# Performance work log

Measured on AMD Instinct MI355X. Metric: run time of the kernel, lower is better.

The kernel has to match this reference:

```python
import jax, jax.numpy as jnp
import numpy as np
import math

N_KEYS = 2048      # set size (number of pragma keys)
EMB = 768          # embed_size
KEY_E = 512        # key_embed_size
VAL_E = 256        # val_embed_size (KEY_E + VAL_E == EMB)
CAT_VOCAB = 100000 # categorical embedding rows
N_REG = 1000       # integer-key embedding rows / per-key Linear(1,256) encoders
HID = 512          # hidden_size (dim_V)
HEADS = 8
N_OUT = 7          # PMA num_outputs
SCALE = math.sqrt(HID)  # original divides by sqrt(dim_V), not sqrt(head_dim)


def _split_heads(x):
    # torch: torch.cat(x.split(dim_V//h, 2), 0)  -> [h*B, N, dim_V/h]
    return jnp.concatenate(jnp.split(x, HEADS, axis=2), axis=0)


def _merge_heads(x):
    # torch: torch.cat(x.split(B, 0), 2)
    return jnp.concatenate(jnp.split(x, HEADS, axis=0), axis=2)


def _mab(Q, K, wq, bq, wk, bk, wv, bv, wo, bo):
    # MAB with ln=False: project, head-split along batch, attend, residual, relu FF residual
    Qp = Q @ wq.T + bq
    Kp = K @ wk.T + bk
    Vp = K @ wv.T + bv
    Q_, K_, V_ = _split_heads(Qp), _split_heads(Kp), _split_heads(Vp)
    A = jax.nn.softmax(jnp.einsum('bqd,bkd->bqk', Q_, K_) / SCALE, axis=-1)
    O = _merge_heads(Q_ + jnp.einsum('bqk,bkd->bqd', A, V_))
    return O + jax.nn.relu(O @ wo.T + bo)


def _forward(reg_values, cat_table, reg_table, reg_W, reg_b,
             q0_w, q0_b, k0_w, k0_b, v0_w, v0_b, o0_w, o0_b,
             qs_w, qs_b, ks_w, ks_b, vs_w, vs_b, os_w, os_b,
             S, pq_w, pq_b, pk_w, pk_b, pv_w, pv_b, po_w, po_b,
             fc_w, fc_b, is_cat, cat_idx, reg_idx):
    # vectorized form of the per-key python loop: gather -> tiny linear encode -> select
    val_emb = reg_W[reg_idx] * reg_values[:, None] + reg_b[reg_idx]     # [N, VAL_E]
    reg_full = jnp.concatenate([reg_table[reg_idx], val_emb], axis=-1)  # [N, EMB]
    emb = jnp.where(is_cat[:, None], cat_table[cat_idx], reg_full)[None]  # [1, N, EMB]
    x = _mab(emb, emb, q0_w, q0_b, k0_w, k0_b, v0_w, v0_b, o0_w, o0_b)
    for i in range(3):
        x = _mab(x, x, qs_w[i], qs_b[i], ks_w[i], ks_b[i], vs_w[i], vs_b[i], os_w[i], os_b[i])
    # decoder: PMA (MAB(S, X)) then Linear(HID, 1)
    s = jnp.broadcast_to(S, (x.shape[0], N_OUT, HID))
    p = _mab(s, x, pq_w, pq_b, pk_w, pk_b, pv_w, pv_b, po_w, po_b)      # [1, N_OUT, HID]
    return (p @ fc_w.T + fc_b).reshape(-1)                              # [N_OUT]


def setup_inputs() -> dict:
    key = jax.random.key(0)
    ks = iter(jax.random.split(key, 48))
    def w(shape, s=0.02):
        return jax.random.normal(next(ks), shape, jnp.float32) * s
    inp = {}
    inp['is_cat'] = jax.random.bernoulli(next(ks), 0.5, (N_KEYS,))
    inp['cat_idx'] = jax.random.randint(next(ks), (N_KEYS,), 0, CAT_VOCAB)
    inp['reg_idx'] = jax.random.randint(next(ks), (N_KEYS,), 0, N_REG)
    inp['reg_values'] = jax.random.uniform(next(ks), (N_KEYS,), jnp.float32, 1.0, 64.0)
    inp['cat_table'] = w((CAT_VOCAB, EMB), 0.05)
    inp['reg_table'] = w((N_REG, KEY_E), 0.05)
    inp['reg_W'] = w((N_REG, VAL_E))
    inp['reg_b'] = w((N_REG, VAL_E))
    inp['q0_w'] = w((HID, EMB)); inp['q0_b'] = w((HID,))
    inp['k0_w'] = w((HID, EMB)); inp['k0_b'] = w((HID,))
    inp['v0_w'] = w((HID, EMB)); inp['v0_b'] = w((HID,))
    inp['o0_w'] = w((HID, HID)); inp['o0_b'] = w((HID,))
    for nm in ['qs', 'ks', 'vs', 'os']:
        inp[nm + '_w'] = w((3, HID, HID))
        inp[nm + '_b'] = w((3, HID))
    inp['S'] = w((1, N_OUT, HID), 0.05)
    for nm in ['pq', 'pk', 'pv', 'po']:
        inp[nm + '_w'] = w((HID, HID))
        inp[nm + '_b'] = w((HID,))
    inp['fc_w'] = w((1, HID)); inp['fc_b'] = w((1,))
    return inp


def reference(is_cat, cat_idx, reg_idx, reg_values, cat_table, reg_table, reg_W, reg_b,
              q0_w, q0_b, k0_w, k0_b, v0_w, v0_b, o0_w, o0_b,
              qs_w, qs_b, ks_w, ks_b, vs_w, vs_b, os_w, os_b,
              S, pq_w, pq_b, pk_w, pk_b, pv_w, pv_b, po_w, po_b, fc_w, fc_b):
    return _forward(reg_values, cat_table, reg_table, reg_W, reg_b,
                    q0_w, q0_b, k0_w, k0_b, v0_w, v0_b, o0_w, o0_b,
                    qs_w, qs_b, ks_w, ks_b, vs_w, vs_b, os_w, os_b,
                    S, pq_w, pq_b, pk_w, pk_b, pv_w, pv_b, po_w, po_b,
                    fc_w, fc_b, is_cat, cat_idx, reg_idx)
```

## Files before the change

### kernel.cpp

```cpp
#include <hip/hip_runtime.h>
#include <hip/hip_bf16.h>
#include <stdint.h>


#define HID 512
#define EMBD 768
#define NCTX 2048
#define HD 64

typedef __attribute__((ext_vector_type(8))) short v8s;
typedef __attribute__((ext_vector_type(4))) float v4f;

#define MFMA(a, b, c) __builtin_amdgcn_mfma_f32_16x16x32_bf16((a), (b), (c), 0, 0, 0)

__device__ __forceinline__ short f2bf(float f) {
  return __builtin_bit_cast(short, __float2bfloat16(f));
}
__device__ __forceinline__ float bf2f(short s) {
  uint32_t u = ((uint32_t)(uint16_t)s) << 16;
  return __builtin_bit_cast(float, u);
}
__device__ __forceinline__ v8s ldbf8(const short* p) { return *(const v8s*)p; }

struct ConvDesc {
  const float* src[20];
  unsigned cum[21];
};

#define NB_CONV 22016u
#define NB_EMB 6144u
#define NB_S 128u

__global__ __launch_bounds__(256) void k_prep(
    ConvDesc d, short* __restrict__ Wdst,
    const int* __restrict__ is_cat, const int* __restrict__ cat_idx,
    const int* __restrict__ reg_idx, const float* __restrict__ reg_values,
    const float* __restrict__ cat_table, const float* __restrict__ reg_table,
    const float* __restrict__ reg_W, const float* __restrict__ reg_b,
    short* __restrict__ emb_out, const float* __restrict__ S,
    short* __restrict__ s_out) {
  unsigned b = blockIdx.x;
  if (b < NB_CONV) {
    unsigned i = b * 256u + threadIdx.x;
    if (i >= d.cum[20]) return;
    int t = 0;
    while (i >= d.cum[t + 1]) ++t;
    Wdst[i] = f2bf(d.src[t][i - d.cum[t]]);
  } else if (b < NB_CONV + NB_EMB) {
    int i = (int)(b - NB_CONV) * 256 + threadIdx.x;
    int n = i / EMBD, e = i - n * EMBD;
    float v;
    if (is_cat[n]) {
      v = cat_table[(long)cat_idx[n] * EMBD + e];
    } else {
      int r = reg_idx[n];
      if (e < 512) v = reg_table[r * 512 + e];
      else {
        int e2 = e - 512;
        v = reg_W[r * 256 + e2] * reg_values[n] + reg_b[r * 256 + e2];
      }
    }
    emb_out[i] = f2bf(v);
  } else {
    int i = (int)(b - NB_CONV - NB_EMB) * 256 + threadIdx.x;
    int row = i >> 9;
    s_out[i] = (row < 7) ? f2bf(S[i]) : (short)0;
  }
}

struct GemmJob {
  const short* A;
  const short* B;
  const float* biasA;
  const float* biasB;
  short* out;
  int N, KK, epi, gx, base;
  float sA, sB;
};
struct GemmBatch {
  GemmJob j[3];
  int nj;
};

__global__ __launch_bounds__(64) void k_gemm_multi(GemmBatch gb) {
  int wg = blockIdx.x;
  int ji = 0;
  if (gb.nj > 1 && wg >= gb.j[1].base) ji = 1;
  if (gb.nj > 2 && wg >= gb.j[2].base) ji = 2;
  const GemmJob& j = gb.j[ji];
  int rel = wg - j.base;
  int bx = rel % j.gx, by = rel / j.gx;
  int l = threadIdx.x, l16 = l & 15, quad = l >> 4;
  int i0 = by * 32, n0 = bx * 64;
  const int KK = j.KK;
  const short* a0p = j.A + (i0 + l16) * KK + quad * 8;
  const short* a1p = a0p + 16 * KK;
  const short* bp = j.B + (n0 + l16) * KK + quad * 8;
  v4f acc[2][4];
  for (int g = 0; g < 2; ++g)
    for (int t = 0; t < 4; ++t) acc[g][t] = (v4f){0.f, 0.f, 0.f, 0.f};
#pragma unroll 4
  for (int k = 0; k < KK; k += 32) {
    v8s a0 = ldbf8(a0p + k);
    v8s a1 = ldbf8(a1p + k);
#pragma unroll
    for (int t = 0; t < 4; ++t) {
      v8s b = ldbf8(bp + t * 16 * KK + k);
      acc[0][t] = MFMA(a0, b, acc[0][t]);
      acc[1][t] = MFMA(a1, b, acc[1][t]);
    }
  }
  for (int g = 0; g < 2; ++g)
    for (int t = 0; t < 4; ++t) {
      int col = n0 + t * 16 + l16;
      float bc = 0.f, sc = 1.f;
      if (j.epi == 0) {
        bc = (col < 512) ? j.biasA[col] : j.biasB[col - 512];
        sc = (col < 512) ? j.sA : j.sB;
      }
      for (int r = 0; r < 4; ++r) {
        int row = i0 + g * 16 + quad * 4 + r;
        float v = acc[g][t][r];
        v = (j.epi == 0) ? (v + bc) * sc : v + j.biasA[row];
        j.out[row * j.N + col] = f2bf(v);
      }
    }
}

template <int KK>
__global__ __launch_bounds__(64) void k_gemm_ff(const short* __restrict__ A,
                                               const short* __restrict__ B,
                                               const float* __restrict__ biasA,
                                               const short* __restrict__ resid,
                                               short* __restrict__ out, int N) {
  int l = threadIdx.x, l16 = l & 15, quad = l >> 4;
  int i0 = blockIdx.y * 32, n0 = blockIdx.x * 64;
  const short* a0p = A + (i0 + l16) * KK + quad * 8;
  const short* a1p = a0p + 16 * KK;
  const short* bp = B + (n0 + l16) * KK + quad * 8;
  v4f acc[2][4];
  for (int g = 0; g < 2; ++g)
    for (int t = 0; t < 4; ++t) acc[g][t] = (v4f){0.f, 0.f, 0.f, 0.f};
#pragma unroll 4
  for (int k = 0; k < KK; k += 32) {
    v8s a0 = ldbf8(a0p + k);
    v8s a1 = ldbf8(a1p + k);
#pragma unroll
    for (int t = 0; t < 4; ++t) {
      v8s b = ldbf8(bp + t * 16 * KK + k);
      acc[0][t] = MFMA(a0, b, acc[0][t]);
      acc[1][t] = MFMA(a1, b, acc[1][t]);
    }
  }
  for (int g = 0; g < 2; ++g)
    for (int t = 0; t < 4; ++t) {
      int col = n0 + t * 16 + l16;
      float bc = biasA[col];
      for (int r = 0; r < 4; ++r) {
        int row = i0 + g * 16 + quad * 4 + r;
        float v = bf2f(resid[row * N + col]) + fmaxf(acc[g][t][r] + bc, 0.f);
        out[row * N + col] = f2bf(v);
      }
    }
}

__global__ __launch_bounds__(256) void k_flash(const short* __restrict__ Q, int qstride,
                                               const short* __restrict__ Kp, int kstride,
                                               const short* __restrict__ Vt,
                                               float* __restrict__ opart,
                                               float* __restrict__ lspart) {
  __shared__ __align__(16) short Kt[64 * 64];
  __shared__ __align__(16) short Vtl[64 * 64];
  __shared__ __align__(16) short P[4][16 * 72];
  const int tid = threadIdx.x;
  const int wave = tid >> 6, l = tid & 63, l16 = l & 15, quad = l >> 4;
  const int h = blockIdx.y, D0 = h * HD;
  const int i0 = blockIdx.x * 64 + wave * 16;
  const int z = blockIdx.z, jbase = z * (NCTX / 4);

  const short* qrow = Q + (i0 + l16) * qstride + D0 + quad * 8;
  const v8s aq0 = ldbf8(qrow);
  const v8s aq1 = ldbf8(qrow + 32);

  const int sr = tid >> 2, sc0 = tid & 3, sc1 = sc0 + 4;
  const short* kg = Kp + (jbase + sr) * kstride + D0;
  const short* vg = Vt + (D0 + sr) * NCTX + jbase;
  short* kl0 = &Kt[(sr * 8 + (sc0 ^ (sr & 7))) * 8];
  short* kl1 = &Kt[(sr * 8 + (sc1 ^ (sr & 7))) * 8];
  short* vl0 = &Vtl[(sr * 8 + (sc0 ^ (sr & 7))) * 8];
  short* vl1 = &Vtl[(sr * 8 + (sc1 ^ (sr & 7))) * 8];

  v4f o[4];
  float lsum[4];
  for (int t = 0; t < 4; ++t) o[t] = (v4f){0.f, 0.f, 0.f, 0.f};
  for (int r = 0; r < 4; ++r) lsum[r] = 0.f;

  v8s pk0 = ldbf8(kg + sc0 * 8), pk1 = ldbf8(kg + sc1 * 8);
  v8s pv0 = ldbf8(vg + sc0 * 8), pv1 = ldbf8(vg + sc1 * 8);

  for (int j0 = 0; j0 < NCTX / 4; j0 += 64) {
    __syncthreads();
    *(v8s*)kl0 = pk0; *(v8s*)kl1 = pk1;
    *(v8s*)vl0 = pv0; *(v8s*)vl1 = pv1;
    __syncthreads();
    int jn = j0 + 64;
    if (jn < NCTX / 4) {
      pk0 = ldbf8(kg + jn * kstride + sc0 * 8);
      pk1 = ldbf8(kg + jn * kstride + sc1 * 8);
      pv0 = ldbf8(vg + jn + sc0 * 8);
      pv1 = ldbf8(vg + jn + sc1 * 8);
    }
    v4f s[4];
#pragma unroll
    for (int kt = 0; kt < 4; ++kt) {
      int R = kt * 16 + l16;
      v8s kb0 = *(const v8s*)&Kt[(R * 8 + (quad ^ (R & 7))) * 8];
      v8s kb1 = *(const v8s*)&Kt[(R * 8 + ((quad + 4) ^ (R & 7))) * 8];
      v4f t0 = (v4f){0.f, 0.f, 0.f, 0.f};
      t0 = MFMA(aq0, kb0, t0);
      s[kt] = MFMA(aq1, kb1, t0);
    }
    short* pw = &P[wave][0];
#pragma unroll
    for (int kt = 0; kt < 4; ++kt)
      for (int r = 0; r < 4; ++r) {
        float p = exp2f(fminf(s[kt][r], 40.f));
        lsum[r] += p;
        pw[(quad * 4 + r) * 72 + kt * 16 + l16] = f2bf(p);
      }
    asm volatile("s_waitcnt lgkmcnt(0)" ::: "memory");
    v8s pa0 = *(const v8s*)&pw[l16 * 72 + quad * 8];
    v8s pa1 = *(const v8s*)&pw[l16 * 72 + 32 + quad * 8];
#pragma unroll
    for (int t = 0; t < 4; ++t) {
      int R = t * 16 + l16;
      v8s bv0 = *(const v8s*)&Vtl[(R * 8 + (quad ^ (R & 7))) * 8];
      v8s bv1 = *(const v8s*)&Vtl[(R * 8 + ((quad + 4) ^ (R & 7))) * 8];
      o[t] = MFMA(pa0, bv0, o[t]);
      o[t] = MFMA(pa1, bv1, o[t]);
    }
  }
  for (int r = 0; r < 4; ++r) {
    lsum[r] += __shfl_xor(lsum[r], 1);
    lsum[r] += __shfl_xor(lsum[r], 2);
    lsum[r] += __shfl_xor(lsum[r], 4);
    lsum[r] += __shfl_xor(lsum[r], 8);
  }
  float* ob = opart + (size_t)z * (NCTX * HID);
  for (int t = 0; t < 4; ++t)
    for (int r = 0; r < 4; ++r)
      ob[(i0 + quad * 4 + r) * HID + D0 + t * 16 + l16] = o[t][r];
  if (l16 == 0)
    for (int r = 0; r < 4; ++r)
      lspart[z * (8 * NCTX) + h * NCTX + i0 + quad * 4 + r] = lsum[r];
}

__global__ void k_combine(const float* __restrict__ op, const float* __restrict__ ls,
                          const short* __restrict__ Qr, int qstride,
                          short* __restrict__ out) {
  const int PS = NCTX * HID;
  int i = blockIdx.x * 256 + threadIdx.x;
  int row = i >> 9, col = i & 511, h = col >> 6;
  float o = op[i] + op[i + PS] + op[i + 2 * PS] + op[i + 3 * PS];
  int li = h * NCTX + row;
  float d = ls[li] + ls[li + 8 * NCTX] + ls[li + 16 * NCTX] + ls[li + 24 * NCTX];
  out[i] = f2bf(bf2f(Qr[row * qstride + col]) + o / d);
}

__global__ __launch_bounds__(64) void k_fc(const short* __restrict__ P,
                                           const float* __restrict__ fcw,
                                           const float* __restrict__ fcb,
                                           float* __restrict__ out) {
  int j = blockIdx.x, l = threadIdx.x;
  float s = 0.f;
  int d0 = l * 8;
  for (int d = d0; d < d0 + 8; ++d) s += bf2f(P[j * HID + d]) * fcw[d];
  for (int msk = 1; msk < 64; msk <<= 1) s += __shfl_xor(s, msk);
  if (l == 0) out[j] = s + fcb[0];
}

extern "C" void kernel_launch(void* const* d_in, const int* in_sizes, int n_in,
                              void* d_out, int out_size, void* d_ws, size_t ws_size,
                              hipStream_t stream) {
  const int* is_cat = (const int*)d_in[0];
  const int* cat_idx = (const int*)d_in[1];
  const int* reg_idx = (const int*)d_in[2];
  const float* reg_values = (const float*)d_in[3];
  const float* cat_table = (const float*)d_in[4];
  const float* reg_table = (const float*)d_in[5];
  const float* reg_W = (const float*)d_in[6];
  const float* reg_b = (const float*)d_in[7];
  const float* q0_w = (const float*)d_in[8];  const float* q0_b = (const float*)d_in[9];
  const float* k0_w = (const float*)d_in[10]; const float* k0_b = (const float*)d_in[11];
  const float* v0_w = (const float*)d_in[12]; const float* v0_b = (const float*)d_in[13];
  const float* o0_w = (const float*)d_in[14]; const float* o0_b = (const float*)d_in[15];
  const float* qs_w = (const float*)d_in[16]; const float* qs_b = (const float*)d_in[17];
  const float* ks_w = (const float*)d_in[18]; const float* ks_b = (const float*)d_in[19];
  const float* vs_w = (const float*)d_in[20]; const float* vs_b = (const float*)d_in[21];
  const float* os_w = (const float*)d_in[22]; const float* os_b = (const float*)d_in[23];
  const float* S    = (const float*)d_in[24];
  const float* pq_w = (const float*)d_in[25]; const float* pq_b = (const float*)d_in[26];
  const float* pk_w = (const float*)d_in[27]; const float* pk_b = (const float*)d_in[28];
  const float* pv_w = (const float*)d_in[29]; const float* pv_b = (const float*)d_in[30];
  const float* po_w = (const float*)d_in[31]; const float* po_b = (const float*)d_in[32];
  const float* fc_w = (const float*)d_in[33]; const float* fc_b = (const float*)d_in[34];

  short* W = (short*)d_ws;

  const unsigned OWQK[4] = {0u, 1441792u, 2490368u, 3538944u};
  const unsigned OWV[4]  = {786432u, 1966080u, 3014656u, 4063232u};
  const unsigned OWO[4]  = {1179648u, 2228224u, 3276800u, 4325376u};
  const unsigned OPQW = 4587520u, OPKW = 4849664u, OPVW = 5111808u, OPOW = 5373952u;
  const unsigned TOTW = 5636096u;
  const unsigned OEMB = TOTW;
  const unsigned OXA  = OEMB + 1572864u;
  const unsigned OXB  = OXA + 1048576u;
  const unsigned OQK  = OXB + 1048576u;
  const unsigned OVT  = OQK + 2097152u;
  const unsigned OOH  = OVT + 1048576u;
  const unsigned OSB  = OOH + 1048576u;
  const unsigned OQPP = OSB + 32768u;
  const unsigned OKPP = OQPP + 32768u;
  const unsigned OOHP = OKPP + 1048576u;
  const unsigned OPP  = OOHP + 32768u;
  const unsigned OF32 = OPP + 32768u;
  float* F = (float*)(W + OF32);
  float* LS = F + 4u * 1048576u;

  const float C2 = 0.06375872f;

  ConvDesc cd;
  const float* srcs[20] = {
      q0_w, k0_w, v0_w, o0_w,
      qs_w, ks_w, vs_w, os_w,
      qs_w + 262144, ks_w + 262144, vs_w + 262144, os_w + 262144,
      qs_w + 524288, ks_w + 524288, vs_w + 524288, os_w + 524288,
      pq_w, pk_w, pv_w, po_w};
  const unsigned cums[21] = {0u,       393216u,  786432u,  1179648u, 1441792u,
                             1703936u, 1966080u, 2228224u, 2490368u, 2752512u,
                             3014656u, 3276800u, 3538944u, 3801088u, 4063232u,
                             4325376u, 4587520u, 4849664u, 5111808u, 5373952u,
                             5636096u};
  for (int i = 0; i < 20; ++i) cd.src[i] = srcs[i];
  for (int i = 0; i < 21; ++i) cd.cum[i] = cums[i];
  k_prep<<<NB_CONV + NB_EMB + NB_S, 256, 0, stream>>>(
      cd, W, is_cat, cat_idx, reg_idx, reg_values, cat_table, reg_table,
      reg_W, reg_b, W + OEMB, S, W + OSB);

  const float* bq[4] = {q0_b, qs_b, qs_b + 512, qs_b + 1024};
  const float* bk[4] = {k0_b, ks_b, ks_b + 512, ks_b + 1024};
  const float* bv[4] = {v0_b, vs_b, vs_b + 512, vs_b + 1024};
  const float* bo[4] = {o0_b, os_b, os_b + 512, os_b + 1024};
  const unsigned oxin[4]  = {OEMB, OXA, OXB, OXA};
  const unsigned oxout[4] = {OXA, OXB, OXA, OXB};

  dim3 gf(32, 8, 4);

  for (int l = 0; l < 4; ++l) {
    const short* X = W + oxin[l];
    short* Xout = W + oxout[l];
    int KKl = (l == 0) ? 768 : 512;
    GemmBatch gb{};
    gb.nj = 2;
    gb.j[0] = {X, W + OWQK[l], bq[l], bk[l], W + OQK, 1024, KKl, 0, 16, 0, 1.f, C2};
    gb.j[1] = {W + OWV[l], X, bv[l], nullptr, W + OVT, 2048, KKl, 1, 32, 1024, 1.f, 1.f};
    k_gemm_multi<<<1536, 64, 0, stream>>>(gb);
    k_flash<<<gf, 256, 0, stream>>>(W + OQK, 1024, W + OQK + 512, 1024, W + OVT, F, LS);
    k_combine<<<(2048 * 512) / 256, 256, 0, stream>>>(F, LS, W + OQK, 1024, W + OOH);
    k_gemm_ff<512><<<dim3(8, 64), 64, 0, stream>>>(W + OOH, W + OWO[l], bo[l], W + OOH, Xout, 512);
  }

  GemmBatch gp{};
  gp.nj = 3;
  gp.j[0] = {W + OSB, W + OPQW, pq_b, pq_b, W + OQPP, 512, 512, 0, 8, 0, 1.f, 1.f};
  gp.j[1] = {W + OXB, W + OPKW, pk_b, pk_b, W + OKPP, 512, 512, 0, 8, 16, C2, C2};
  gp.j[2] = {W + OPVW, W + OXB, pv_b, nullptr, W + OVT, 2048, 512, 1, 32, 528, 1.f, 1.f};
  k_gemm_multi<<<1040, 64, 0, stream>>>(gp);
  k_flash<<<dim3(1, 8, 4), 256, 0, stream>>>(W + OQPP, 512, W + OKPP, 512, W + OVT, F, LS);
  k_combine<<<(16 * 512) / 256, 256, 0, stream>>>(F, LS, W + OQPP, 512, W + OOHP);
  k_gemm_ff<512><<<dim3(8, 1), 64, 0, stream>>>(W + OOHP, W + OPOW, po_b, W + OOHP, W + OPP, 512);
  k_fc<<<7, 64, 0, stream>>>(W + OPP, fc_w, fc_b, (float*)d_out);
}
```

Baseline: 728.0 us.

## Fuse split-K flash combine into flash kernel via last-arriving-block reduction

```diff
diff --git a/kernel.cpp b/kernel.cpp
--- a/kernel.cpp
+++ b/kernel.cpp
@@ -38,7 +38,7 @@
     const float* __restrict__ cat_table, const float* __restrict__ reg_table,
     const float* __restrict__ reg_W, const float* __restrict__ reg_b,
     short* __restrict__ emb_out, const float* __restrict__ S,
-    short* __restrict__ s_out) {
+    short* __restrict__ s_out, int* __restrict__ cnt) {
   unsigned b = blockIdx.x;
   if (b < NB_CONV) {
     unsigned i = b * 256u + threadIdx.x;
@@ -61,10 +61,12 @@
       }
     }
     emb_out[i] = f2bf(v);
-  } else {
+  } else if (b < NB_CONV + NB_EMB + NB_S) {
     int i = (int)(b - NB_CONV - NB_EMB) * 256 + threadIdx.x;
     int row = i >> 9;
     s_out[i] = (row < 7) ? f2bf(S[i]) : (short)0;
+  } else {
+    for (int k = 0; k < 8; ++k) cnt[threadIdx.x * 8 + k] = 0;
   }
 }
 
@@ -168,10 +170,13 @@
                                                const short* __restrict__ Kp, int kstride,
                                                const short* __restrict__ Vt,
                                                float* __restrict__ opart,
-                                               float* __restrict__ lspart) {
+                                               float* __restrict__ lspart,
+                                               int* __restrict__ cnt,
+                                               short* __restrict__ oout) {
   __shared__ __align__(16) short Kt[64 * 64];
   __shared__ __align__(16) short Vtl[64 * 64];
   __shared__ __align__(16) short P[4][16 * 72];
+  __shared__ int arrival;
   const int tid = threadIdx.x;
   const int wave = tid >> 6, l = tid & 63, l16 = l & 15, quad = l >> 4;
   const int h = blockIdx.y, D0 = h * HD;
@@ -253,18 +258,34 @@
   if (l16 == 0)
     for (int r = 0; r < 4; ++r)
       lspart[z * (8 * NCTX) + h * NCTX + i0 + quad * 4 + r] = lsum[r];
-}
-
-__global__ void k_combine(const float* __restrict__ op, const float* __restrict__ ls,
-                          const short* __restrict__ Qr, int qstride,
-                          short* __restrict__ out) {
-  const int PS = NCTX * HID;
-  int i = blockIdx.x * 256 + threadIdx.x;
-  int row = i >> 9, col = i & 511, h = col >> 6;
-  float o = op[i] + op[i + PS] + op[i + 2 * PS] + op[i + 3 * PS];
-  int li = h * NCTX + row;
-  float d = ls[li] + ls[li + 8 * NCTX] + ls[li + 16 * NCTX] + ls[li + 24 * NCTX];
-  out[i] = f2bf(bf2f(Qr[row * qstride + col]) + o / d);
+
+  __threadfence();
+  __syncthreads();
+  if (tid == 0) arrival = atomicAdd(&cnt[blockIdx.y * gridDim.x + blockIdx.x], 1);
+  __syncthreads();
+  if (arrival != 3) return;
+  __threadfence();
+
+  float dtot[4];
+#pragma unroll
+  for (int r = 0; r < 4; ++r) {
+    float d = 0.f;
+    for (int zz = 0; zz < 4; ++zz)
+      d += (zz == z) ? lsum[r]
+                     : lspart[zz * (8 * NCTX) + h * NCTX + i0 + quad * 4 + r];
+    dtot[r] = d;
+  }
+#pragma unroll
+  for (int t = 0; t < 4; ++t)
+    for (int r = 0; r < 4; ++r) {
+      int grow = i0 + quad * 4 + r;
+      int gcol = D0 + t * 16 + l16;
+      float osum = 0.f;
+      for (int zz = 0; zz < 4; ++zz)
+        osum += (zz == z) ? o[t][r]
+                          : opart[(size_t)zz * (NCTX * HID) + grow * HID + gcol];
+      oout[grow * HID + gcol] = f2bf(bf2f(Q[grow * qstride + gcol]) + osum / dtot[r]);
+    }
 }
 
 __global__ __launch_bounds__(64) void k_fc(const short* __restrict__ P,
@@ -326,6 +347,7 @@
   const unsigned OF32 = OPP + 32768u;
   float* F = (float*)(W + OF32);
   float* LS = F + 4u * 1048576u;
+  int* CNT = (int*)(LS + 4u * 8u * NCTX);
 
   const float C2 = 0.06375872f;
 
@@ -343,9 +365,9 @@
                              5636096u};
   for (int i = 0; i < 20; ++i) cd.src[i] = srcs[i];
   for (int i = 0; i < 21; ++i) cd.cum[i] = cums[i];
-  k_prep<<<NB_CONV + NB_EMB + NB_S, 256, 0, stream>>>(
+  k_prep<<<NB_CONV + NB_EMB + NB_S + 1, 256, 0, stream>>>(
       cd, W, is_cat, cat_idx, reg_idx, reg_values, cat_table, reg_table,
-      reg_W, reg_b, W + OEMB, S, W + OSB);
+      reg_W, reg_b, W + OEMB, S, W + OSB, CNT);
 
   const float* bq[4] = {q0_b, qs_b, qs_b + 512, qs_b + 1024};
   const float* bk[4] = {k0_b, ks_b, ks_b + 512, ks_b + 1024};
@@ -365,8 +387,8 @@
     gb.j[0] = {X, W + OWQK[l], bq[l], bk[l], W + OQK, 1024, KKl, 0, 16, 0, 1.f, C2};
     gb.j[1] = {W + OWV[l], X, bv[l], nullptr, W + OVT, 2048, KKl, 1, 32, 1024, 1.f, 1.f};
     k_gemm_multi<<<1536, 64, 0, stream>>>(gb);
-    k_flash<<<gf, 256, 0, stream>>>(W + OQK, 1024, W + OQK + 512, 1024, W + OVT, F, LS);
-    k_combine<<<(2048 * 512) / 256, 256, 0, stream>>>(F, LS, W + OQK, 1024, W + OOH);
+    k_flash<<<gf, 256, 0, stream>>>(W + OQK, 1024, W + OQK + 512, 1024, W + OVT,
+                                    F, LS, CNT + l * 256, W + OOH);
     k_gemm_ff<512><<<dim3(8, 64), 64, 0, stream>>>(W + OOH, W + OWO[l], bo[l], W + OOH, Xout, 512);
   }
 
@@ -376,8 +398,8 @@
   gp.j[1] = {W + OXB, W + OPKW, pk_b, pk_b, W + OKPP, 512, 512, 0, 8, 16, C2, C2};
   gp.j[2] = {W + OPVW, W + OXB, pv_b, nullptr, W + OVT, 2048, 512, 1, 32, 528, 1.f, 1.f};
   k_gemm_multi<<<1040, 64, 0, stream>>>(gp);
-  k_flash<<<dim3(1, 8, 4), 256, 0, stream>>>(W + OQPP, 512, W + OKPP, 512, W + OVT, F, LS);
-  k_combine<<<(16 * 512) / 256, 256, 0, stream>>>(F, LS, W + OQPP, 512, W + OOHP);
+  k_flash<<<dim3(1, 8, 4), 256, 0, stream>>>(W + OQPP, 512, W + OKPP, 512, W + OVT,
+                                             F, LS, CNT + 4 * 256, W + OOHP);
   k_gemm_ff<512><<<dim3(8, 1), 64, 0, stream>>>(W + OOHP, W + OPOW, po_b, W + OOHP, W + OPP, 512);
   k_fc<<<7, 64, 0, stream>>>(W + OPP, fc_w, fc_b, (float*)d_out);
 }
```

New measurement: 1.283 ms. 1.76x slower.
